# Kernel optimization log

Measured on AMD Instinct MI355X. Metric: run time of the kernel, lower is better.

Reference implementation:

```python
import jax, jax.numpy as jnp
import numpy as np

B, Z, DEG = 4096, 128, 16   # batch (dtPt), totalZONES, avg out-degree
E = Z * DEG                 # number of directed edges = number of tiny MLPs
WV = 0.1                    # WEIGHT_VARIANCE stand-in for normal_(0, WV) init


def setup_inputs() -> dict:
    key = jax.random.key(0)
    ks = jax.random.split(key, 7)
    x = jax.random.normal(ks[0], (B, Z), dtype=jnp.float32)
    # simple graph: each src zone has DEG distinct neighbors (no duplicate edges)
    rng = np.random.default_rng(0)
    dst = np.argsort(rng.random((Z, Z)), axis=1)[:, :DEG].reshape(-1)
    src = np.repeat(np.arange(Z), DEG)
    W1 = jax.random.normal(ks[1], (E, 2, 4), dtype=jnp.float32) * WV
    b1 = jax.random.normal(ks[2], (E, 4), dtype=jnp.float32) * WV
    W2 = jax.random.normal(ks[3], (E, 4, 4), dtype=jnp.float32) * WV
    b2 = jax.random.normal(ks[4], (E, 4), dtype=jnp.float32) * WV
    W3 = jax.random.normal(ks[5], (E, 4), dtype=jnp.float32) * WV  # Linear(4,1) weight, squeezed
    b3 = jax.random.normal(ks[6], (E,), dtype=jnp.float32) * WV
    return {"x": x, "dtPt": B,
            "src": jnp.asarray(src, jnp.int32), "dst": jnp.asarray(dst, jnp.int32),
            "W1": W1, "b1": b1, "W2": W2, "b2": b2, "W3": W3, "b3": b3}


def reference(x, dtPt, src, dst, W1, b1, W2, b2, W3, b3):
    # gather per-edge pair features: [B, E, 2]
    h = jnp.stack([x[:, src], x[:, dst]], axis=-1)
    # per-edge tiny MLP as batched GEMMs (one fused op over all E edges)
    h = jnp.tanh(jnp.einsum('bei,eio->beo', h, W1) + b1)   # [B, E, 4]
    h = jnp.tanh(jnp.einsum('bei,eio->beo', h, W2) + b2)   # [B, E, 4]
    beta = jax.nn.sigmoid(jnp.einsum('bei,ei->be', h, W3) + b3)  # [B, E]
    # scatter into ones-initialized adjacency output [B, Z, Z]
    out = jnp.ones((x.shape[0], Z, Z), dtype=x.dtype)
    return out.at[:, src, dst].set(beta)
```

## Files before the change

### kernel.cpp

```cpp
#include <hip/hip_runtime.h>


#define ZONES 128
#define DEG   16
#define NB    8

__global__ __launch_bounds__(256) void fused_edge_mlp(
    const float* __restrict__ x,
    const int*   __restrict__ dst,
    const float* __restrict__ W1,
    const float* __restrict__ b1,
    const float* __restrict__ W2,
    const float* __restrict__ b2,
    const float* __restrict__ W3,
    const float* __restrict__ b3,
    float* __restrict__ out)
{
    __shared__ float buf[2 * 8 * ZONES];

    const int tid  = threadIdx.x;
    const int rg   = blockIdx.x;
    const int b0   = blockIdx.y * NB;

    const int boff = tid >> 7;
    const int t    = tid & 127;
    const int e    = rg * 128 + t;
    const int srow = rg * 8 + (t >> 4);
    const int dcol = dst[e];

    float w1[8], b1v[4], w2[16], b2v[4], w3[4];
    #pragma unroll
    for (int i = 0; i < 8; ++i)  w1[i]  = W1[e * 8 + i];
    #pragma unroll
    for (int i = 0; i < 4; ++i)  b1v[i] = b1[e * 4 + i];
    #pragma unroll
    for (int i = 0; i < 16; ++i) w2[i]  = W2[e * 16 + i];
    #pragma unroll
    for (int i = 0; i < 4; ++i)  b2v[i] = b2[e * 4 + i];
    #pragma unroll
    for (int i = 0; i < 4; ++i)  w3[i]  = W3[e * 4 + i];
    const float b3s = b3[e];

    float4* f4buf = reinterpret_cast<float4*>(buf);
    float4* out4  = reinterpret_cast<float4*>(out);
    const float4 ones4 = make_float4(1.f, 1.f, 1.f, 1.f);

    #pragma unroll
    for (int it = 0; it < NB / 2; ++it) {
        const int b = b0 + it * 2 + boff;

        f4buf[tid]       = ones4;
        f4buf[tid + 256] = ones4;
        __syncthreads();

        const float xs = x[b * ZONES + srow];
        const float xd = x[b * ZONES + dcol];

        float h1[4];
        #pragma unroll
        for (int o = 0; o < 4; ++o)
            h1[o] = tanhf(fmaf(xs, w1[o], fmaf(xd, w1[4 + o], b1v[o])));

        float h2[4];
        #pragma unroll
        for (int o = 0; o < 4; ++o) {
            float z = b2v[o];
            #pragma unroll
            for (int k = 0; k < 4; ++k)
                z = fmaf(h1[k], w2[k * 4 + o], z);
            h2[o] = tanhf(z);
        }

        float z = b3s;
        #pragma unroll
        for (int o = 0; o < 4; ++o)
            z = fmaf(h2[o], w3[o], z);
        const float beta = 1.0f / (1.0f + __expf(-z));

        buf[boff * 1024 + (t >> 4) * 128 + dcol] = beta;
        __syncthreads();

        #pragma unroll
        for (int bb = 0; bb < 2; ++bb) {
            const int bw = b0 + it * 2 + bb;
            out4[(size_t)bw * (ZONES * ZONES / 4) + rg * 256 + tid] =
                f4buf[bb * 256 + tid];
        }
        __syncthreads();
    }
}

extern "C" void kernel_launch(void* const* d_in, const int* in_sizes, int n_in,
                              void* d_out, int out_size, void* d_ws, size_t ws_size,
                              hipStream_t stream) {
    const float* x   = (const float*)d_in[0];
    const int*   dst = (const int*)  d_in[3];
    const float* W1  = (const float*)d_in[4];
    const float* b1  = (const float*)d_in[5];
    const float* W2  = (const float*)d_in[6];
    const float* b2  = (const float*)d_in[7];
    const float* W3  = (const float*)d_in[8];
    const float* b3  = (const float*)d_in[9];
    float* out = (float*)d_out;

    const int B = in_sizes[0] / ZONES;
    dim3 grid(ZONES / 8, B / NB);
    fused_edge_mlp<<<grid, 256, 0, stream>>>(x, dst, W1, b1, W2, b2, W3, b3, out);
}
```

Baseline: 51.43 us.

## Double-buffer shared tile, init ones once, use fast tanh/sigmoid, larger batch per block

Each block now covers 32 batches instead of 8, which spreads the per-edge weight loads over more work. The shared staging tile is double-buffered and filled with ones only once. Each thread rewrites the same slot every iteration, so the rest of the tile stays at one, and this drops the re-init and two of the three barriers per iteration. Weight loads are vectorized to float4, and tanh and sigmoid use exp plus hardware reciprocal approximations instead of precise library calls. The costs are fewer blocks in the grid and slightly reduced accuracy in the activations.

```diff
diff --git a/kernel.cpp b/kernel.cpp
--- a/kernel.cpp
+++ b/kernel.cpp
@@ -2,8 +2,15 @@
 
 
 #define ZONES 128
-#define DEG   16
-#define NB    8
+#define NB    32
+
+__device__ __forceinline__ float fast_tanh(float v) {
+    float e = __expf(2.0f * v);
+    return 1.0f - 2.0f * __builtin_amdgcn_rcpf(e + 1.0f);
+}
+__device__ __forceinline__ float fast_sigmoid(float v) {
+    return __builtin_amdgcn_rcpf(1.0f + __expf(-v));
+}
 
 __global__ __launch_bounds__(256) void fused_edge_mlp(
     const float* __restrict__ x,
@@ -16,7 +23,7 @@
     const float* __restrict__ b3,
     float* __restrict__ out)
 {
-    __shared__ float buf[2 * 8 * ZONES];
+    __shared__ float buf[2][2][8 * ZONES];
 
     const int tid  = threadIdx.x;
     const int rg   = blockIdx.x;
@@ -29,29 +36,30 @@
     const int dcol = dst[e];
 
     float w1[8], b1v[4], w2[16], b2v[4], w3[4];
-    #pragma unroll
-    for (int i = 0; i < 8; ++i)  w1[i]  = W1[e * 8 + i];
-    #pragma unroll
-    for (int i = 0; i < 4; ++i)  b1v[i] = b1[e * 4 + i];
-    #pragma unroll
-    for (int i = 0; i < 16; ++i) w2[i]  = W2[e * 16 + i];
-    #pragma unroll
-    for (int i = 0; i < 4; ++i)  b2v[i] = b2[e * 4 + i];
-    #pragma unroll
-    for (int i = 0; i < 4; ++i)  w3[i]  = W3[e * 4 + i];
+    *(float4*)&w1[0]  = ((const float4*)(W1 + e * 8))[0];
+    *(float4*)&w1[4]  = ((const float4*)(W1 + e * 8))[1];
+    *(float4*)&b1v[0] = ((const float4*)(b1 + e * 4))[0];
+    *(float4*)&w2[0]  = ((const float4*)(W2 + e * 16))[0];
+    *(float4*)&w2[4]  = ((const float4*)(W2 + e * 16))[1];
+    *(float4*)&w2[8]  = ((const float4*)(W2 + e * 16))[2];
+    *(float4*)&w2[12] = ((const float4*)(W2 + e * 16))[3];
+    *(float4*)&b2v[0] = ((const float4*)(b2 + e * 4))[0];
+    *(float4*)&w3[0]  = ((const float4*)(W3 + e * 4))[0];
     const float b3s = b3[e];
 
-    float4* f4buf = reinterpret_cast<float4*>(buf);
-    float4* out4  = reinterpret_cast<float4*>(out);
+    float4* f4 = (float4*)buf;
     const float4 ones4 = make_float4(1.f, 1.f, 1.f, 1.f);
+    #pragma unroll
+    for (int i = 0; i < 4; ++i) f4[tid + 256 * i] = ones4;
+    __syncthreads();
 
-    #pragma unroll
+    float4* out4 = (float4*)out;
+    const int scat = boff ? -1 : (t >> 4) * 128 + dcol;
+
+    #pragma unroll 4
     for (int it = 0; it < NB / 2; ++it) {
+        const int p = it & 1;
         const int b = b0 + it * 2 + boff;
-
-        f4buf[tid]       = ones4;
-        f4buf[tid + 256] = ones4;
-        __syncthreads();
 
         const float xs = x[b * ZONES + srow];
         const float xd = x[b * ZONES + dcol];
@@ -59,7 +67,7 @@
         float h1[4];
         #pragma unroll
         for (int o = 0; o < 4; ++o)
-            h1[o] = tanhf(fmaf(xs, w1[o], fmaf(xd, w1[4 + o], b1v[o])));
+            h1[o] = fast_tanh(fmaf(xs, w1[o], fmaf(xd, w1[4 + o], b1v[o])));
 
         float h2[4];
         #pragma unroll
@@ -68,26 +76,26 @@
             #pragma unroll
             for (int k = 0; k < 4; ++k)
                 z = fmaf(h1[k], w2[k * 4 + o], z);
-            h2[o] = tanhf(z);
+            h2[o] = fast_tanh(z);
         }
 
         float z = b3s;
         #pragma unroll
         for (int o = 0; o < 4; ++o)
             z = fmaf(h2[o], w3[o], z);
-        const float beta = 1.0f / (1.0f + __expf(-z));
+        const float beta = fast_sigmoid(z);
 
-        buf[boff * 1024 + (t >> 4) * 128 + dcol] = beta;
+        buf[p][boff][(t >> 4) * 128 + dcol] = beta;
         __syncthreads();
 
         #pragma unroll
         for (int bb = 0; bb < 2; ++bb) {
             const int bw = b0 + it * 2 + bb;
             out4[(size_t)bw * (ZONES * ZONES / 4) + rg * 256 + tid] =
-                f4buf[bb * 256 + tid];
+                ((float4*)buf[p][bb])[tid];
         }
-        __syncthreads();
     }
+    (void)scat;
 }
 
 extern "C" void kernel_launch(void* const* d_in, const int* in_sizes, int n_in,
```

Result: no change. 50.61 us (-1.6%).
